# Kernel tuning notes

Hardware: AMD Instinct MI355X
Metric: run time of the kernel (lower is better)

## Reference

```python
import jax, jax.numpy as jnp
import numpy as np
import math

B, T, D = 4, 2048, 1024
H, DH = 16, 64  # n_heads, d_head; H*DH == D


def setup_inputs() -> dict:
    key = jax.random.key(0)
    ks = jax.random.split(key, 5)
    s = 0.02
    return {
        "x": jax.random.normal(ks[0], (B, T, D), dtype=jnp.float32),
        "W_qkv": jax.random.normal(ks[1], (D, 3 * D), dtype=jnp.float32) * s,
        "b_qkv": jnp.zeros((3 * D,), dtype=jnp.float32),
        "W_out": jax.random.normal(ks[2], (D, D), dtype=jnp.float32) * s,
        "b_out": jnp.zeros((D,), dtype=jnp.float32),
    }


def reference(x, W_qkv, b_qkv, W_out, b_out):
    Bx, Tx, Cx = x.shape
    qkv = x @ W_qkv + b_qkv                      # [B,T,3D]
    q, k, v = jnp.split(qkv, 3, axis=-1)
    q = q.reshape(Bx, Tx, H, DH).transpose(0, 2, 1, 3)  # [B,H,T,dh]
    k = k.reshape(Bx, Tx, H, DH).transpose(0, 2, 1, 3)
    v = v.reshape(Bx, Tx, H, DH).transpose(0, 2, 1, 3)
    scores = jnp.einsum("bhqd,bhkd->bhqk", q, k) / math.sqrt(DH)
    causal = jnp.tril(jnp.ones((Tx, Tx), dtype=bool))
    scores = jnp.where(causal, scores, jnp.float32(-jnp.inf))
    attn = jax.nn.softmax(scores, axis=-1)       # dropout p=0.0 -> identity
    out = jnp.einsum("bhqk,bhkd->bhqd", attn, v)
    out = out.transpose(0, 2, 1, 3).reshape(Bx, Tx, Cx)
    return out @ W_out + b_out
```

## Files before the change

kernel.cpp:

```cpp
#include <hip/hip_runtime.h>

#define DEVI __device__ __forceinline__

typedef __attribute__((ext_vector_type(8))) short short8;
typedef __attribute__((ext_vector_type(4))) float floatx4;

typedef const __attribute__((address_space(1))) void* gbl_ptr_t;
typedef __attribute__((address_space(3))) void* lds_ptr_t;

DEVI unsigned short f2bf(float f) {
  union { float f; unsigned int u; } v; v.f = f;
  unsigned int r = v.u + 0x7fffu + ((v.u >> 16) & 1u);
  return (unsigned short)(r >> 16);
}

DEVI unsigned int cvt_pk_bf16(float a, float b) {
  unsigned int r;
  asm("v_cvt_pk_bf16_f32 %0, %1, %2" : "=v"(r) : "v"(a), "v"(b));
  return r;
}

constexpr int Bc = 4, Tc = 2048, Dc = 1024, Hc = 16, DHc = 64;
constexpr int Mrows = Bc * Tc;
constexpr long PLANE = (long)Bc * Hc * Tc * DHc;

__global__ __launch_bounds__(256) void cast_f32_bf16(const float* __restrict__ in,
                                                     unsigned short* __restrict__ out, int n4) {
  int i = blockIdx.x * 256 + threadIdx.x;
  if (i < n4) {
    float4 v = ((const float4*)in)[i];
    ushort4 o;
    o.x = f2bf(v.x); o.y = f2bf(v.y); o.z = f2bf(v.z); o.w = f2bf(v.w);
    ((ushort4*)out)[i] = o;
  }
}

__global__ __launch_bounds__(256) void transpose_cast(const float* __restrict__ in,
                                                      unsigned short* __restrict__ out,
                                                      int K, int N) {
  __shared__ float tile[32][33];
  int bx = blockIdx.x * 32;
  int by = blockIdx.y * 32;
  int tx = threadIdx.x & 31, ty = threadIdx.x >> 5;
#pragma unroll
  for (int i = ty; i < 32; i += 8) tile[i][tx] = in[(long)(by + i) * N + bx + tx];
  __syncthreads();
#pragma unroll
  for (int i = ty; i < 32; i += 8) out[(long)(bx + i) * K + by + tx] = f2bf(tile[tx][i]);
}

template <int MODE>
__global__ __launch_bounds__(256) void gemm_bt(const unsigned short* __restrict__ A,
                                               const unsigned short* __restrict__ Bt,
                                               const float* __restrict__ bias,
                                               void* __restrict__ Cout,
                                               int M, int N, int K) {
  constexpr int BK = 64;
  __shared__ __align__(16) short As[128 * 64];
  __shared__ __align__(16) short Bs[128 * 64];

  const int tid = threadIdx.x;
  const int wave = tid >> 6;
  const int lane = tid & 63;
  const int l16 = lane & 15;
  const int quad = lane >> 4;
  const int wm = (wave >> 1) * 64;
  const int wn = (wave & 1) * 64;
  const int rsub = lane >> 3;
  const int csub = (lane & 7) * 8;

  int nwg = gridDim.x * gridDim.y;
  int lin = blockIdx.y * gridDim.x + blockIdx.x;
  if ((nwg & 7) == 0) {
    int cpx = nwg >> 3;
    lin = (lin & 7) * cpx + (lin >> 3);
  }
  const int bx = lin % gridDim.x;
  const int by = lin / gridDim.x;

  const long row0 = (long)by * 128;
  const long col0 = (long)bx * 128;

  floatx4 acc[4][4];
#pragma unroll
  for (int i = 0; i < 4; i++)
#pragma unroll
    for (int j = 0; j < 4; j++) acc[i][j] = (floatx4){0.f, 0.f, 0.f, 0.f};

  for (int k0 = 0; k0 < K; k0 += BK) {
#pragma unroll
    for (int c = 0; c < 4; c++) {
      int rb = (c * 4 + wave) * 8;
      const unsigned short* sA = &A[(row0 + rb + rsub) * (long)K + k0 + csub];
      __builtin_amdgcn_global_load_lds((gbl_ptr_t)sA, (lds_ptr_t)&As[rb * 64], 16, 0, 0);
      const unsigned short* sB = &Bt[(col0 + rb + rsub) * (long)K + k0 + csub];
      __builtin_amdgcn_global_load_lds((gbl_ptr_t)sB, (lds_ptr_t)&Bs[rb * 64], 16, 0, 0);
    }
    __syncthreads();
#pragma unroll
    for (int kk = 0; kk < BK; kk += 32) {
      short8 af[4], bfr[4];
#pragma unroll
      for (int mt = 0; mt < 4; mt++)
        af[mt] = *(const short8*)&As[(wm + mt * 16 + l16) * 64 + kk + quad * 8];
#pragma unroll
      for (int nt = 0; nt < 4; nt++)
        bfr[nt] = *(const short8*)&Bs[(wn + nt * 16 + l16) * 64 + kk + quad * 8];
#pragma unroll
      for (int mt = 0; mt < 4; mt++)
#pragma unroll
        for (int nt = 0; nt < 4; nt++)
          acc[mt][nt] = __builtin_amdgcn_mfma_f32_16x16x32_bf16(af[mt], bfr[nt], acc[mt][nt], 0, 0, 0);
    }
    __syncthreads();
  }

#pragma unroll
  for (int mt = 0; mt < 4; mt++)
#pragma unroll
    for (int nt = 0; nt < 4; nt++)
#pragma unroll
      for (int r = 0; r < 4; r++) {
        long row = row0 + wm + mt * 16 + quad * 4 + r;
        long col = col0 + wn + nt * 16 + l16;
        float v = acc[mt][nt][r] + bias[col];
        if (MODE == 0) {
          int which = (int)(col >> 10);
          int hc = (int)col & 1023;
          int h = hc >> 6, d = hc & 63;
          int b = (int)(row >> 11), t = (int)row & 2047;
          ((unsigned short*)Cout)[(long)which * PLANE +
                                  (((long)(b * Hc + h) * Tc + t) << 6) + d] = f2bf(v);
        } else {
          ((float*)Cout)[row * N + col] = v;
        }
      }
}

__global__ __launch_bounds__(256, 8) void flash_attn(const unsigned short* __restrict__ qkv,
                                                     unsigned short* __restrict__ attn_out) {
  constexpr int PD = 72;
  __shared__ __align__(16) short Ks[64 * PD];
  __shared__ __align__(16) short Vts[64 * PD];
  __shared__ __align__(16) short Ps[4 * 16 * PD];

  const int tid = threadIdx.x;
  const int wave = tid >> 6;
  const int lane = tid & 63;
  const int l16 = lane & 15;
  const int quad = lane >> 4;

  const int lin = blockIdx.y * 32 + blockIdx.x;
  const int lin2 = (lin & 7) * 256 + (lin >> 3);
  const int bh = lin2 >> 5;
  const int qx = 31 - (lin2 & 31);

  const long base = (long)bh * Tc * DHc;
  const unsigned short* Qg = qkv + base;
  const unsigned short* Kg = qkv + PLANE + base;
  const unsigned short* Vg = qkv + 2 * PLANE + base;
  const int b = bh >> 4, h = bh & 15;

  constexpr float CEXP = 0.125f * 1.44269504f;
  short* Pw = &Ps[wave * 16 * PD];

  const int kr = tid >> 3;
  const int kc = (tid & 7) * 8;

  const int q0 = qx * 64 + wave * 16;

  short8 qf[2];
#pragma unroll
  for (int kk = 0; kk < 2; kk++)
    qf[kk] = *(const short8*)&Qg[(long)(q0 + l16) * 64 + kk * 32 + quad * 8];

  floatx4 oacc[4];
#pragma unroll
  for (int j = 0; j < 4; j++) oacc[j] = (floatx4){0.f, 0.f, 0.f, 0.f};
  float lpart = 0.f;

  const int ntiles = qx + 1;

  uint4 Kreg[2], Vreg[2];
  Kreg[0] = *(const uint4*)&Kg[(long)kr * 64 + kc];
  Kreg[1] = *(const uint4*)&Kg[(long)(32 + kr) * 64 + kc];
  Vreg[0] = *(const uint4*)&Vg[(long)lane * 64 + wave * 8];
  Vreg[1] = *(const uint4*)&Vg[(long)lane * 64 + (wave + 4) * 8];

#pragma unroll 1
  for (int kt = 0; kt < ntiles; kt++) {
    __syncthreads();
    *(uint4*)&Ks[kr * PD + kc] = Kreg[0];
    *(uint4*)&Ks[(32 + kr) * PD + kc] = Kreg[1];
#pragma unroll
    for (int c = 0; c < 2; c++) {
      int dc = wave + 4 * c;
      unsigned short vb[8];
      *(uint4*)vb = Vreg[c];
#pragma unroll
      for (int j = 0; j < 8; j++) Vts[(dc * 8 + j) * PD + lane] = (short)vb[j];
    }
    __syncthreads();
    if (kt + 1 < ntiles) {
      long koff = (long)(kt + 1) * 64;
      Kreg[0] = *(const uint4*)&Kg[(koff + kr) * 64 + kc];
      Kreg[1] = *(const uint4*)&Kg[(koff + 32 + kr) * 64 + kc];
    }

    floatx4 sacc[4];
#pragma unroll
    for (int j = 0; j < 4; j++) sacc[j] = (floatx4){0.f, 0.f, 0.f, 0.f};
#pragma unroll
    for (int kk = 0; kk < 2; kk++) {
      short8 kf[4];
#pragma unroll
      for (int nt = 0; nt < 4; nt++)
        kf[nt] = *(const short8*)&Ks[(nt * 16 + l16) * PD + kk * 32 + quad * 8];
#pragma unroll
      for (int nt = 0; nt < 4; nt++)
        sacc[nt] = __builtin_amdgcn_mfma_f32_16x16x32_bf16(kf[nt], qf[kk], sacc[nt], 0, 0, 0);
    }

    if (kt == qx) {
      const int qi = q0 + l16;
#pragma unroll
      for (int nt = 0; nt < 4; nt++) {
#pragma unroll
        for (int r = 0; r < 4; r++) {
          int ki = kt * 64 + nt * 16 + quad * 4 + r;
          if (ki > qi) sacc[nt][r] = -3.0e38f;
        }
      }
    }

#pragma unroll
    for (int nt = 0; nt < 4; nt++) {
      float p0 = exp2f(sacc[nt][0] * CEXP);
      float p1 = exp2f(sacc[nt][1] * CEXP);
      float p2 = exp2f(sacc[nt][2] * CEXP);
      float p3 = exp2f(sacc[nt][3] * CEXP);
      lpart += (p0 + p1) + (p2 + p3);
      uint2 w;
      w.x = cvt_pk_bf16(p0, p1);
      w.y = cvt_pk_bf16(p2, p3);
      *(uint2*)&Pw[l16 * PD + nt * 16 + quad * 4] = w;
    }

    if (kt + 1 < ntiles) {
      long koff = (long)(kt + 1) * 64;
      Vreg[0] = *(const uint4*)&Vg[(koff + lane) * 64 + wave * 8];
      Vreg[1] = *(const uint4*)&Vg[(koff + lane) * 64 + (wave + 4) * 8];
    }

#pragma unroll
    for (int kk = 0; kk < 2; kk++) {
      short8 pf = *(const short8*)&Pw[l16 * PD + kk * 32 + quad * 8];
      short8 vf[4];
#pragma unroll
      for (int dt = 0; dt < 4; dt++)
        vf[dt] = *(const short8*)&Vts[(dt * 16 + l16) * PD + kk * 32 + quad * 8];
#pragma unroll
      for (int dt = 0; dt < 4; dt++)
        oacc[dt] = __builtin_amdgcn_mfma_f32_16x16x32_bf16(pf, vf[dt], oacc[dt], 0, 0, 0);
    }
  }

  float l = lpart;
  l += __shfl_xor(l, 16);
  l += __shfl_xor(l, 32);
#pragma unroll
  for (int r = 0; r < 4; r++) {
    float lr = __shfl(l, quad * 4 + r);
    float inv = 1.0f / lr;
    int t = q0 + quad * 4 + r;
#pragma unroll
    for (int dt = 0; dt < 4; dt++) {
      int d = dt * 16 + l16;
      attn_out[(((long)(b * Tc + t) * Hc + h) << 6) + d] = f2bf(oacc[dt][r] * inv);
    }
  }
}

extern "C" void kernel_launch(void* const* d_in, const int* in_sizes, int n_in,
                              void* d_out, int out_size, void* d_ws, size_t ws_size,
                              hipStream_t stream) {
  const float* x = (const float*)d_in[0];
  const float* Wqkv = (const float*)d_in[1];
  const float* bqkv = (const float*)d_in[2];
  const float* Wout = (const float*)d_in[3];
  const float* bout = (const float*)d_in[4];

  char* ws = (char*)d_ws;
  unsigned short* x_bf   = (unsigned short*)ws;
  unsigned short* wqkv_t = (unsigned short*)(ws + 16777216);
  unsigned short* wout_t = (unsigned short*)(ws + 16777216 + 6291456);
  unsigned short* qkv    = (unsigned short*)(ws + 25165824);
  unsigned short* attn   = x_bf;

  cast_f32_bf16<<<dim3(Mrows * Dc / 4 / 256), dim3(256), 0, stream>>>(x, x_bf, Mrows * Dc / 4);
  transpose_cast<<<dim3(3 * Dc / 32, Dc / 32), dim3(256), 0, stream>>>(Wqkv, wqkv_t, Dc, 3 * Dc);
  transpose_cast<<<dim3(Dc / 32, Dc / 32), dim3(256), 0, stream>>>(Wout, wout_t, Dc, Dc);

  gemm_bt<0><<<dim3(3 * Dc / 128, Mrows / 128), dim3(256), 0, stream>>>(
      x_bf, wqkv_t, bqkv, qkv, Mrows, 3 * Dc, Dc);

  flash_attn<<<dim3(32, Bc * Hc), dim3(256), 0, stream>>>(qkv, attn);

  gemm_bt<1><<<dim3(Dc / 128, Mrows / 128), dim3(256), 0, stream>>>(
      attn, wout_t, bout, d_out, Mrows, Dc, Dc);
}
```

Before: 338.8 us.

## Double-buffer K/V tiles in LDS with XOR swizzle, one barrier per tile

Moves the flash-attention K/V staging to two LDS buffers. The next tile is written into the alternate buffer while the current one is consumed, and global loads are prefetched two tiles ahead. This cuts the per-iteration barriers from two to one. Padded LDS rows are replaced by an XOR swizzle to avoid bank conflicts. LDS use grows from about 27 KB to 40 KB per block, which may reduce occupancy against the launch bound of 8 blocks.

```diff
diff --git a/kernel.cpp b/kernel.cpp
--- a/kernel.cpp
+++ b/kernel.cpp
@@ -19,6 +19,8 @@
   asm("v_cvt_pk_bf16_f32 %0, %1, %2" : "=v"(r) : "v"(a), "v"(b));
   return r;
 }
+
+DEVI int swz(int i) { return i ^ ((i >> 3) & 56); }
 
 constexpr int Bc = 4, Tc = 2048, Dc = 1024, Hc = 16, DHc = 64;
 constexpr int Mrows = Bc * Tc;
@@ -139,10 +141,9 @@
 
 __global__ __launch_bounds__(256, 8) void flash_attn(const unsigned short* __restrict__ qkv,
                                                      unsigned short* __restrict__ attn_out) {
-  constexpr int PD = 72;
-  __shared__ __align__(16) short Ks[64 * PD];
-  __shared__ __align__(16) short Vts[64 * PD];
-  __shared__ __align__(16) short Ps[4 * 16 * PD];
+  __shared__ __align__(16) short Ks[2 * 64 * 64];
+  __shared__ __align__(16) short Vts[2 * 64 * 64];
+  __shared__ __align__(16) short Ps[4 * 16 * 64];
 
   const int tid = threadIdx.x;
   const int wave = tid >> 6;
@@ -162,7 +163,6 @@
   const int b = bh >> 4, h = bh & 15;
 
   constexpr float CEXP = 0.125f * 1.44269504f;
-  short* Pw = &Ps[wave * 16 * PD];
 
   const int kr = tid >> 3;
   const int kc = (tid & 7) * 8;
@@ -186,39 +186,63 @@
   Kreg[1] = *(const uint4*)&Kg[(long)(32 + kr) * 64 + kc];
   Vreg[0] = *(const uint4*)&Vg[(long)lane * 64 + wave * 8];
   Vreg[1] = *(const uint4*)&Vg[(long)lane * 64 + (wave + 4) * 8];
-
-#pragma unroll 1
-  for (int kt = 0; kt < ntiles; kt++) {
-    __syncthreads();
-    *(uint4*)&Ks[kr * PD + kc] = Kreg[0];
-    *(uint4*)&Ks[(32 + kr) * PD + kc] = Kreg[1];
+  {
+    *(uint4*)&Ks[swz(kr * 64 + kc)] = Kreg[0];
+    *(uint4*)&Ks[swz((32 + kr) * 64 + kc)] = Kreg[1];
 #pragma unroll
     for (int c = 0; c < 2; c++) {
       int dc = wave + 4 * c;
       unsigned short vb[8];
       *(uint4*)vb = Vreg[c];
 #pragma unroll
-      for (int j = 0; j < 8; j++) Vts[(dc * 8 + j) * PD + lane] = (short)vb[j];
-    }
-    __syncthreads();
+      for (int j = 0; j < 8; j++) Vts[swz((dc * 8 + j) * 64 + lane)] = (short)vb[j];
+    }
+  }
+  if (ntiles > 1) {
+    Kreg[0] = *(const uint4*)&Kg[(long)(64 + kr) * 64 + kc];
+    Kreg[1] = *(const uint4*)&Kg[(long)(96 + kr) * 64 + kc];
+    Vreg[0] = *(const uint4*)&Vg[(long)(64 + lane) * 64 + wave * 8];
+    Vreg[1] = *(const uint4*)&Vg[(long)(64 + lane) * 64 + (wave + 4) * 8];
+  }
+  __syncthreads();
+
+#pragma unroll 1
+  for (int kt = 0; kt < ntiles; kt++) {
+    const int cb = (kt & 1) << 12;
+    const int nb = cb ^ 4096;
+
+    floatx4 sacc[4];
+#pragma unroll
+    for (int j = 0; j < 4; j++) sacc[j] = (floatx4){0.f, 0.f, 0.f, 0.f};
+#pragma unroll
+    for (int kk = 0; kk < 2; kk++) {
+      short8 kf[4];
+#pragma unroll
+      for (int nt = 0; nt < 4; nt++)
+        kf[nt] = *(const short8*)&Ks[swz(cb + (nt * 16 + l16) * 64 + kk * 32 + quad * 8)];
+#pragma unroll
+      for (int nt = 0; nt < 4; nt++)
+        sacc[nt] = __builtin_amdgcn_mfma_f32_16x16x32_bf16(kf[nt], qf[kk], sacc[nt], 0, 0, 0);
+    }
+
     if (kt + 1 < ntiles) {
-      long koff = (long)(kt + 1) * 64;
+      *(uint4*)&Ks[swz(nb + kr * 64 + kc)] = Kreg[0];
+      *(uint4*)&Ks[swz(nb + (32 + kr) * 64 + kc)] = Kreg[1];
+#pragma unroll
+      for (int c = 0; c < 2; c++) {
+        int dc = wave + 4 * c;
+        unsigned short vb[8];
+        *(uint4*)vb = Vreg[c];
+#pragma unroll
+        for (int j = 0; j < 8; j++) Vts[swz(nb + (dc * 8 + j) * 64 + lane)] = (short)vb[j];
+      }
+    }
+    if (kt + 2 < ntiles) {
+      long koff = (long)(kt + 2) * 64;
       Kreg[0] = *(const uint4*)&Kg[(koff + kr) * 64 + kc];
       Kreg[1] = *(const uint4*)&Kg[(koff + 32 + kr) * 64 + kc];
-    }
-
-    floatx4 sacc[4];
-#pragma unroll
-    for (int j = 0; j < 4; j++) sacc[j] = (floatx4){0.f, 0.f, 0.f, 0.f};
-#pragma unroll
-    for (int kk = 0; kk < 2; kk++) {
-      short8 kf[4];
-#pragma unroll
-      for (int nt = 0; nt < 4; nt++)
-        kf[nt] = *(const short8*)&Ks[(nt * 16 + l16) * PD + kk * 32 + quad * 8];
-#pragma unroll
-      for (int nt = 0; nt < 4; nt++)
-        sacc[nt] = __builtin_amdgcn_mfma_f32_16x16x32_bf16(kf[nt], qf[kk], sacc[nt], 0, 0, 0);
+      Vreg[0] = *(const uint4*)&Vg[(koff + lane) * 64 + wave * 8];
+      Vreg[1] = *(const uint4*)&Vg[(koff + lane) * 64 + (wave + 4) * 8];
     }
 
     if (kt == qx) {
@@ -243,26 +267,22 @@
       uint2 w;
       w.x = cvt_pk_bf16(p0, p1);
       w.y = cvt_pk_bf16(p2, p3);
-      *(uint2*)&Pw[l16 * PD + nt * 16 + quad * 4] = w;
-    }
-
-    if (kt + 1 < ntiles) {
-      long koff = (long)(kt + 1) * 64;
-      Vreg[0] = *(const uint4*)&Vg[(koff + lane) * 64 + wave * 8];
-      Vreg[1] = *(const uint4*)&Vg[(koff + lane) * 64 + (wave + 4) * 8];
+      *(uint2*)&Ps[swz(wave * 1024 + l16 * 64 + nt * 16 + quad * 4)] = w;
     }
 
 #pragma unroll
     for (int kk = 0; kk < 2; kk++) {
-      short8 pf = *(const short8*)&Pw[l16 * PD + kk * 32 + quad * 8];
+      short8 pf = *(const short8*)&Ps[swz(wave * 1024 + l16 * 64 + kk * 32 + quad * 8)];
       short8 vf[4];
 #pragma unroll
       for (int dt = 0; dt < 4; dt++)
-        vf[dt] = *(const short8*)&Vts[(dt * 16 + l16) * PD + kk * 32 + quad * 8];
+        vf[dt] = *(const short8*)&Vts[swz(cb + (dt * 16 + l16) * 64 + kk * 32 + quad * 8)];
 #pragma unroll
       for (int dt = 0; dt < 4; dt++)
         oacc[dt] = __builtin_amdgcn_mfma_f32_16x16x32_bf16(pf, vf[dt], oacc[dt], 0, 0, 0);
     }
+
+    if (kt + 1 < ntiles) __syncthreads();
   }
 
   float l = lpart;
```

Measured after the change: 336.7 us. No clear change (-0.6%).
